# Kernel optimization log

Hardware: AMD Instinct MI355X
Metric: run time of the kernel (lower is better)

## Reference

```python
import jax, jax.numpy as jnp
import numpy as np

B, N, DIM, H, DH, K = 4, 2048, 512, 6, 64, 16
KEEP_PROB = 0.9  # 1 - dropout_rate
LOG2PI = float(np.log(2.0 * np.pi))
LOG_PRIOR = float(np.log(1.0 / K))


def setup_inputs() -> dict:
    key = jax.random.key(0)
    ks = jax.random.split(key, 7)
    inputs_q = jax.random.normal(ks[0], (B, N, DIM), dtype=jnp.float32)
    # decoder-style causal mask, shape [B, 1, q_len, kv_len]
    causal = jnp.tril(jnp.ones((N, N), dtype=jnp.float32))
    mask = jnp.broadcast_to(causal[None, None], (B, 1, N, N))
    # dropout keep mask broadcast across the query dim: [B, H, 1, kv_len]
    keep = jax.random.bernoulli(ks[1], KEEP_PROB, (B, H, 1, N)).astype(jnp.float32)
    w_qkv = jax.random.normal(ks[2], (DIM, 3 * H * DH), dtype=jnp.float32) * 0.02
    w_out = jax.random.normal(ks[3], (H * DH, DIM), dtype=jnp.float32) * 0.02
    mu_lookup = jax.random.normal(ks[4], (K, DIM), dtype=jnp.float32)
    logvar_lookup = jax.random.normal(ks[5], (K, DIM), dtype=jnp.float32) * 0.1
    return {
        "inputs_q": inputs_q,
        "mask": mask,
        "keep": keep,
        "w_qkv": w_qkv,
        "w_out": w_out,
        "mu_lookup": mu_lookup,
        "logvar_lookup": logvar_lookup,
    }


def reference(inputs_q, mask, keep, w_qkv, w_out, mu_lookup, logvar_lookup):
    # --- MultiHeadDotProductAttention (self-attn path) ---
    qkv = (inputs_q @ w_qkv).reshape(B, N, 3, H, DH)  # [B,N,3,H,DH]
    q, k, v = qkv[:, :, 0], qkv[:, :, 1], qkv[:, :, 2]
    # bias: 0 where mask > 0, -1e10 elsewhere (note: no 1/sqrt(d) scaling, as in source)
    bias = jnp.where(mask > 0, 0.0, -1e10)
    attn_weights = jnp.einsum('bqhd,bkhd->bhqk', q, k) + bias  # [B,H,N,N]
    attn_weights = jax.nn.softmax(attn_weights, axis=-1)
    # broadcast dropout: mask shared across the query dim
    attn_weights = attn_weights * keep / KEEP_PROB
    attn_out = jnp.einsum('bhqk,bkhd->bqhd', attn_weights, v)
    attn_out = attn_out.reshape(B, N, H * DH) @ w_out  # [B,N,DIM]

    # --- GMM posterior approx q(y|x) ~= p(y|z) (approx_qy_x, vectorized over k) ---
    z = attn_out.mean(axis=1)  # pooled latent, [B,DIM]
    diff = z[:, None, :] - mu_lookup[None]  # [B,K,DIM]
    llh = -0.5 * jnp.sum(
        diff * diff / jnp.exp(logvar_lookup)[None] + logvar_lookup[None] + LOG2PI,
        axis=-1,
    )  # [B,K]
    logLogit_qy_x = llh + LOG_PRIOR
    qy_x = jax.nn.softmax(logLogit_qy_x, axis=1)  # [B,K]

    # combine mixture mean back in so both branches are live in one output
    return attn_out + (qy_x @ mu_lookup)[:, None, :]
```

## Files before the change

### kernel.cpp

```cpp
#include <hip/hip_runtime.h>
#include <cstdint>
#include <cstddef>

#define NH 6
#define NSEQ 2048
#define DIMD 512
#define BATCH 4
#define HD 384
#define LOG2PI_F 1.8378770664093453f
#define LOG2E_F 1.4426950408889634f
#define M12L2_F (-17.312340490667562f)

typedef __attribute__((ext_vector_type(8))) short short8;
typedef __attribute__((ext_vector_type(8))) unsigned short ushort8;
typedef __attribute__((ext_vector_type(4))) unsigned short ushort4v;
typedef __attribute__((ext_vector_type(4))) float floatx4;

__device__ inline unsigned short f2bf(float f){
  unsigned int u = __float_as_uint(f);
  u += 0x7FFFu + ((u>>16)&1u);
  return (unsigned short)(u>>16);
}

__device__ inline float exp2_raw(float x){
  float r; asm("v_exp_f32 %0, %1" : "=v"(r) : "v"(x)); return r;
}

#define GLD16(gp, lp) __builtin_amdgcn_global_load_lds( \
  (const __attribute__((address_space(1))) void*)(gp), \
  (__attribute__((address_space(3))) void*)(lp), 16, 0, 0)

__device__ inline void wtrans_body(
    const float* __restrict__ src, unsigned short* __restrict__ dst,
    int R, int C, int bx, int by, unsigned short* Ls, int t)
{
  const int r = t>>2, c0 = (t&3)*16;
  const int d0 = by*64, n0 = bx*64;
  #pragma unroll
  for (int j=0;j<16;j+=4){
    floatx4 v = *(const floatx4*)(src + (size_t)(d0+r)*C + n0 + c0 + j);
    #pragma unroll
    for(int jj=0;jj<4;jj++) Ls[r*72 + c0+j+jj] = f2bf(v[jj]);
  }
  __syncthreads();
  #pragma unroll
  for (int j=0;j<16;j+=8){
    ushort8 o;
    #pragma unroll
    for(int jj=0;jj<8;jj++) o[jj] = Ls[(c0+j+jj)*72 + r];
    *(ushort8*)(dst + (size_t)(n0+r)*R + d0 + c0 + j) = o;
  }
}

__global__ __launch_bounds__(256) void prep(
    const float* __restrict__ xq, unsigned short* __restrict__ xbf,
    const float* __restrict__ w_qkv, unsigned short* __restrict__ wqT,
    const float* __restrict__ w_out, unsigned short* __restrict__ woT)
{
  __shared__ __attribute__((aligned(16))) unsigned short Ls[64*72];
  const int bid = blockIdx.x, t = threadIdx.x;
  if (bid < 4096){
    int i = bid*256 + t;
    floatx4 v = *(const floatx4*)(xq + (size_t)i*4);
    ushort4v r;
    #pragma unroll
    for(int j=0;j<4;j++) r[j] = f2bf(v[j]);
    *(ushort4v*)(xbf + (size_t)i*4) = r;
  } else if (bid < 4240){
    int rb = bid - 4096;
    wtrans_body(w_qkv, wqT, 512, 1152, rb%18, rb/18, Ls, t);
  } else {
    int rb = bid - 4240;
    wtrans_body(w_out, woT, 384, 512, rb%8, rb/8, Ls, t);
  }
}

__global__ __launch_bounds__(256) void gemm_qkv(
    const unsigned short* __restrict__ A,
    const unsigned short* __restrict__ Bt,
    const float* __restrict__ keep,
    unsigned short* __restrict__ Qo, unsigned short* __restrict__ Ko,
    unsigned short* __restrict__ Vt)
{
  __shared__ __attribute__((aligned(16))) unsigned short Cs[128*132];
  unsigned short* As = Cs;
  unsigned short* Bs = Cs + 128*64;
  const int tid = threadIdx.x;
  const int w = tid>>6, lane = tid&63;
  const int wr = w>>1, wc = w&1;
  const int quad = lane>>4, l16 = lane&15;
  const int tM = blockIdx.x*128, tN = blockIdx.y*128;
  const int r8 = lane>>3, c8 = (lane&7)*8;
  floatx4 acc[4][4];
  floatx4 zed = {0.f,0.f,0.f,0.f};
  #pragma unroll
  for (int i=0;i<4;i++)
    #pragma unroll
    for(int j=0;j<4;j++) acc[i][j] = zed;

  for (int k0=0; k0<512; k0+=64){
    #pragma unroll
    for (int i=0;i<4;i++){
      int row = w*32 + i*8;
      GLD16(A  + (size_t)(tM+row+r8)*512 + k0 + c8, As + row*64);
      GLD16(Bt + (size_t)(tN+row+r8)*512 + k0 + c8, Bs + row*64);
    }
    __syncthreads();
    #pragma unroll
    for (int kk=0; kk<64; kk+=32){
      short8 af[4], bf[4];
      #pragma unroll
      for(int mt=0;mt<4;mt++)
        af[mt] = *(const short8*)(As + (wr*64+mt*16+l16)*64 + kk + quad*8);
      #pragma unroll
      for(int nt=0;nt<4;nt++)
        bf[nt] = *(const short8*)(Bs + (wc*64+nt*16+l16)*64 + kk + quad*8);
      #pragma unroll
      for(int mt=0;mt<4;mt++)
        #pragma unroll
        for(int nt=0;nt<4;nt++)
          acc[mt][nt] = __builtin_amdgcn_mfma_f32_16x16x32_bf16(af[mt], bf[nt], acc[mt][nt], 0,0,0);
    }
    __syncthreads();
  }
  #pragma unroll
  for(int mt=0;mt<4;mt++)
    #pragma unroll
    for(int nt=0;nt<4;nt++){
      int gcol = tN + wc*64 + nt*16 + l16;
      float qs = (gcol < 384) ? LOG2E_F : 1.0f;
      #pragma unroll
      for(int r=0;r<4;r++)
        Cs[(wr*64+mt*16+quad*4+r)*132 + wc*64+nt*16+l16] = f2bf(acc[mt][nt][r]*qs);
    }
  __syncthreads();
  if (blockIdx.y < 6){
    const int row = tid>>1, colh = (tid&1)*64;
    const int gcol0 = tN + colh;
    const int t = gcol0/384, rem = gcol0 - t*384, h = rem>>6;
    const int grow = tM + row, b = grow>>11, n = grow & 2047;
    unsigned short* dst = (t==0 ? Qo : Ko) + ((size_t)((b*NH+h)*NSEQ+n))*64;
    #pragma unroll
    for(int j=0;j<8;j++)
      *(ushort8*)(dst + j*8) = *(const ushort8*)(Cs + row*132 + colh + j*8);
  } else {
    const int dcol = tid>>1;
    const int nh   = (tid&1)*64;
    const int gcol = tN + dcol;
    const int rem = gcol - 768, h = rem>>6, dh = rem&63;
    const int b = tM>>11, nb = tM & 2047;
    const float* kp = keep + (size_t)(b*NH+h)*NSEQ + nb + nh;
    unsigned short* dst = Vt + ((size_t)((b*NH+h)*64 + dh))*NSEQ + nb + nh;
    #pragma unroll
    for (int j8=0;j8<8;j8++){
      floatx4 k0 = *(const floatx4*)(kp + j8*8);
      floatx4 k1 = *(const floatx4*)(kp + j8*8 + 4);
      ushort8 o;
      #pragma unroll
      for(int u=0;u<4;u++)
        o[u]   = (k0[u] < 0.5f) ? (unsigned short)0 : Cs[(nh + j8*8 + u)*132 + dcol];
      #pragma unroll
      for(int u=0;u<4;u++)
        o[4+u] = (k1[u] < 0.5f) ? (unsigned short)0 : Cs[(nh + j8*8 + 4 + u)*132 + dcol];
      *(ushort8*)(dst + j8*8) = o;
    }
  }
}

__global__ __launch_bounds__(256, 3) void attn_kernel(
    const unsigned short* __restrict__ Qg, const unsigned short* __restrict__ Kg,
    const unsigned short* __restrict__ VtG,
    unsigned short* __restrict__ atp)
{
  __shared__ __attribute__((aligned(16))) float sm[4*32*34 + 128];
  float* Ocs  = sm;
  float* accs = sm + 4*32*34;
  const int tid = threadIdx.x;
  const int w = tid>>6, lane = tid&63;
  const int quad = lane>>4, l16 = lane&15;
  const int bid = blockIdx.x;
  const int idx = bid>>3;
  const int bh  = (bid&7) + 8*(idx % 3);
  const int c   = 63 - idx/3;
  const int b = bh/NH, h = bh - b*NH;
  const unsigned short* Qb = Qg  + (size_t)bh*NSEQ*64;
  const int q0 = c*32;
  const int nkt = (c>>1) + 1;
  const int q_abs0 = q0 + l16;

  const unsigned short* Kl = Kg  + (size_t)bh*NSEQ*64 + (size_t)l16*64 + quad*8;
  const unsigned short* Vl = VtG + (size_t)bh*64*NSEQ + (size_t)l16*NSEQ + quad*8;

  short8 qf[2][2];
  #pragma unroll
  for(int mt=0;mt<2;mt++)
    #pragma unroll
    for(int kc=0;kc<2;kc++)
      qf[mt][kc] = *(const short8*)(Qb + (size_t)(q0+mt*16+l16)*64 + kc*32 + quad*8);

  floatx4 O[2][4];
  float accl[2] = {0.f, 0.f};
  floatx4 zed = {0.f,0.f,0.f,0.f};
  floatx4 m12v = {M12L2_F, M12L2_F, M12L2_F, M12L2_F};
  #pragma unroll
  for(int mt=0;mt<2;mt++)
    #pragma unroll
    for(int dt=0;dt<4;dt++) O[mt][dt] = zed;

  for (int kt = w; kt < nkt; kt += 4){
    const int kB = kt*64;
    short8 vf[2][4];
    const unsigned short* vp0 = Vl + kB;
    #pragma unroll
    for(int kh=0;kh<2;kh++)
      #pragma unroll
      for(int dt=0;dt<4;dt++)
        vf[kh][dt] = *(const short8*)(vp0 + (size_t)dt*32768 + kh*32);

    floatx4 sacc[2][4];
    #pragma unroll
    for(int mt=0;mt<2;mt++)
      #pragma unroll
      for(int nt=0;nt<4;nt++) sacc[mt][nt] = m12v;
    const unsigned short* kp0 = Kl + (size_t)kt*4096;
    #pragma unroll
    for(int nt=0;nt<4;nt++){
      short8 kf0 = *(const short8*)(kp0 + nt*1024);
      short8 kf1 = *(const short8*)(kp0 + nt*1024 + 32);
      #pragma unroll
      for(int mt=0;mt<2;mt++){
        sacc[mt][nt] = __builtin_amdgcn_mfma_f32_16x16x32_bf16(kf0, qf[mt][0], sacc[mt][nt], 0,0,0);
        sacc[mt][nt] = __builtin_amdgcn_mfma_f32_16x16x32_bf16(kf1, qf[mt][1], sacc[mt][nt], 0,0,0);
      }
    }

    const bool dia = (kt == nkt-1);
    #pragma unroll
    for(int mt=0;mt<2;mt++){
      const int qa = q_abs0 + mt*16;
      unsigned int d0[4], d1[4];
      float rs = 0.f;
      #pragma unroll
      for(int nt=0;nt<4;nt++){
        const int key0 = kB + nt*16 + quad*4;
        float p0 = exp2_raw(sacc[mt][nt][0]);
        float p1 = exp2_raw(sacc[mt][nt][1]);
        float p2 = exp2_raw(sacc[mt][nt][2]);
        float p3 = exp2_raw(sacc[mt][nt][3]);
        if (dia){
          p0 = (key0   <= qa) ? p0 : 0.f;
          p1 = (key0+1 <= qa) ? p1 : 0.f;
          p2 = (key0+2 <= qa) ? p2 : 0.f;
          p3 = (key0+3 <= qa) ? p3 : 0.f;
        }
        rs += (p0+p1) + (p2+p3);
        asm("v_cvt_pk_bf16_f32 %0, %1, %2" : "=v"(d0[nt]) : "v"(p0), "v"(p1));
        asm("v_cvt_pk_bf16_f32 %0, %1, %2" : "=v"(d1[nt]) : "v"(p2), "v"(p3));
      }
      accl[mt] += rs;
      #pragma unroll
      for(int kh=0;kh<2;kh++){
        unsigned int x0 = d0[2*kh],   x1 = d1[2*kh];
        unsigned int y0 = d0[2*kh+1], y1 = d1[2*kh+1];
        asm("v_permlane32_swap_b32 %0, %1" : "+v"(x0), "+v"(y0));
        asm("v_permlane16_swap_b32 %0, %1" : "+v"(x0), "+v"(y0));
        asm("v_permlane32_swap_b32 %0, %1" : "+v"(x1), "+v"(y1));
        asm("v_permlane16_swap_b32 %0, %1" : "+v"(x1), "+v"(y1));
        union { unsigned int u[4]; short8 s; } cvt;
        cvt.u[0] = x0; cvt.u[1] = x1; cvt.u[2] = y0; cvt.u[3] = y1;
        short8 pf = cvt.s;
        #pragma unroll
        for(int dt=0;dt<4;dt++)
          O[mt][dt] = __builtin_amdgcn_mfma_f32_16x16x32_bf16(pf, vf[kh][dt], O[mt][dt], 0,0,0);
      }
    }
  }

  #pragma unroll
  for(int mt=0;mt<2;mt++){
    accl[mt] += __shfl_xor(accl[mt], 16, 64);
    accl[mt] += __shfl_xor(accl[mt], 32, 64);
  }
  if (quad == 0){
    accs[w*32 + l16]      = accl[0];
    accs[w*32 + 16 + l16] = accl[1];
  }

  const int orow = tid>>3, oc4 = (tid&7)*4;
  float sc2 = 0.f;
  #pragma unroll
  for (int h2=0; h2<2; ++h2){
    float* Ow = Ocs + w*(32*34);
    #pragma unroll
    for(int mt=0;mt<2;mt++)
      #pragma unroll
      for(int d2=0;d2<2;d2++){
        const int dt = h2*2 + d2;
        #pragma unroll
        for(int r=0;r<4;r++)
          Ow[(mt*16+quad*4+r)*34 + d2*16 + l16] = O[mt][dt][r];
      }
    __syncthreads();
    if (h2 == 0){
      float as = accs[orow] + accs[32+orow] + accs[64+orow] + accs[96+orow];
      sc2 = (1.0f/0.9f) / as;
    }
    float fv[4];
    #pragma unroll
    for(int j=0;j<4;j++) fv[j] = 0.f;
    #pragma unroll
    for(int s=0;s<4;s++){
      const float* p = Ocs + s*(32*34) + orow*34 + oc4;
      #pragma unroll
      for(int j=0;j<4;j++) fv[j] += p[j];
    }
    ushort4v o4;
    #pragma unroll
    for(int j=0;j<4;j++) o4[j] = f2bf(fv[j]*sc2);
    *(ushort4v*)(atp + ((size_t)(b*NSEQ + q0 + orow))*HD + h*64 + h2*32 + oc4) = o4;
    __syncthreads();
  }
}

__global__ __launch_bounds__(256) void gemm_proj(
    const unsigned short* __restrict__ A,
    const unsigned short* __restrict__ Bt,
    float* __restrict__ out,
    float* __restrict__ z)
{
  __shared__ __attribute__((aligned(16))) unsigned short As[128*64];
  __shared__ __attribute__((aligned(16))) unsigned short Bs[128*64];
  const int tid = threadIdx.x;
  const int w = tid>>6, lane = tid&63;
  const int wr = w>>1, wc = w&1;
  const int quad = lane>>4, l16 = lane&15;
  const int tM = blockIdx.x*128, tN = blockIdx.y*128;
  const int r8 = lane>>3, c8 = (lane&7)*8;
  floatx4 acc[4][4];
  floatx4 zed = {0.f,0.f,0.f,0.f};
  #pragma unroll
  for (int i=0;i<4;i++)
    #pragma unroll
    for(int j=0;j<4;j++) acc[i][j] = zed;

  for (int k0=0; k0<384; k0+=64){
    #pragma unroll
    for (int i=0;i<4;i++){
      int row = w*32 + i*8;
      GLD16(A  + (size_t)(tM+row+r8)*384 + k0 + c8, As + row*64);
      GLD16(Bt + (size_t)(tN+row+r8)*384 + k0 + c8, Bs + row*64);
    }
    __syncthreads();
    #pragma unroll
    for (int kk=0; kk<64; kk+=32){
      short8 af[4], bf[4];
      #pragma unroll
      for(int mt=0;mt<4;mt++)
        af[mt] = *(const short8*)(As + (wr*64+mt*16+l16)*64 + kk + quad*8);
      #pragma unroll
      for(int nt=0;nt<4;nt++)
        bf[nt] = *(const short8*)(Bs + (wc*64+nt*16+l16)*64 + kk + quad*8);
      #pragma unroll
      for(int mt=0;mt<4;mt++)
        #pragma unroll
        for(int nt=0;nt<4;nt++)
          acc[mt][nt] = __builtin_amdgcn_mfma_f32_16x16x32_bf16(af[mt], bf[nt], acc[mt][nt], 0,0,0);
    }
    __syncthreads();
  }
  #pragma unroll
  for(int mt=0;mt<4;mt++){
    int grow = tM + wr*64 + mt*16 + quad*4;
    #pragma unroll
    for(int nt=0;nt<4;nt++){
      int gcol = tN + wc*64 + nt*16 + l16;
      #pragma unroll
      for(int r=0;r<4;r++)
        out[(size_t)(grow+r)*512 + gcol] = acc[mt][nt][r];
    }
  }
  #pragma unroll
  for(int nt=0;nt<4;nt++){
    float s = 0.f;
    #pragma unroll
    for(int mt=0;mt<4;mt++)
      #pragma unroll
      for(int r=0;r<4;r++) s += acc[mt][nt][r];
    s += __shfl_xor(s, 16, 64);
    s += __shfl_xor(s, 32, 64);
    if (quad == 0){
      int gcol = tN + wc*64 + nt*16 + l16;
      atomicAdd(&z[(tM>>11)*DIMD + gcol], s);
    }
  }
}

__global__ __launch_bounds__(256) void gmm_kernel(
    const float* __restrict__ z, const float* __restrict__ mu,
    const float* __restrict__ lv, float* __restrict__ c)
{
  __shared__ float sh[16];
  __shared__ float qy[16];
  int tid = threadIdx.x;
  int k = tid>>4, li = tid&15;
  int b = blockIdx.x;
  float part = 0.f;
  for(int d=li; d<DIMD; d+=16){
    float zz = z[b*DIMD+d] * (1.0f/2048.0f);
    float m = mu[k*DIMD+d], l = lv[k*DIMD+d];
    float diff = zz - m;
    part += diff*diff*__expf(-l) + l + LOG2PI_F;
  }
  #pragma unroll
  for(int off=8;off>=1;off>>=1) part += __shfl_xor(part, off, 64);
  if (li==0) sh[k] = part;
  __syncthreads();
  if (tid<16){
    float logit = -0.5f*sh[tid];
    float mx = logit;
    #pragma unroll
    for(int off=8;off>=1;off>>=1) mx = fmaxf(mx, __shfl_xor(mx, off, 64));
    float e = __expf(logit-mx);
    float se = e;
    #pragma unroll
    for(int off=8;off>=1;off>>=1) se += __shfl_xor(se, off, 64);
    qy[tid] = e/se;
  }
  __syncthreads();
  for(int d=tid; d<DIMD; d+=256){
    float accv = 0.f;
    #pragma unroll
    for(int kk=0;kk<16;kk++) accv += qy[kk]*mu[kk*DIMD+d];
    c[b*DIMD+d] = accv;
  }
}

__global__ __launch_bounds__(256) void final_add(
    float* __restrict__ out, const float* __restrict__ c)
{
  size_t i = ((size_t)blockIdx.x*256 + threadIdx.x)*4;
  int d = (int)(i & 511);
  int b = (int)(i >> 20);
  floatx4 a = *(const floatx4*)(out + i);
  floatx4 cc = *(const floatx4*)(c + b*DIMD + d);
  *(floatx4*)(out + i) = a + cc;
}

extern "C" void kernel_launch(void* const* d_in, const int* in_sizes, int n_in,
                              void* d_out, int out_size, void* d_ws, size_t ws_size,
                              hipStream_t stream) {
  const float* inputs_q = (const float*)d_in[0];
  const float* keep  = (const float*)d_in[2];
  const float* w_qkv = (const float*)d_in[3];
  const float* w_out = (const float*)d_in[4];
  const float* mu    = (const float*)d_in[5];
  const float* lv    = (const float*)d_in[6];
  float* out = (float*)d_out;
  char* ws = (char*)d_ws;
  size_t off = 0;
  auto alloc = [&](size_t bytes){ void* p = ws + off; off += (bytes + 255) & ~(size_t)255; return p; };
  unsigned short* Qb  = (unsigned short*)alloc((size_t)24*2048*64*2);
  unsigned short* Kb  = (unsigned short*)alloc((size_t)24*2048*64*2);
  unsigned short* Vt  = (unsigned short*)alloc((size_t)24*64*2048*2);
  unsigned short* xbf = (unsigned short*)alloc((size_t)8192*512*2);
  unsigned short* wqT = (unsigned short*)alloc((size_t)1152*512*2);
  unsigned short* woT = (unsigned short*)alloc((size_t)512*384*2);
  unsigned short* atp = (unsigned short*)alloc((size_t)8192*384*2);
  float* z  = (float*)alloc((size_t)4*512*4);
  float* c  = (float*)alloc((size_t)4*512*4);

  hipMemsetAsync(z, 0, 4*512*4, stream);
  prep<<<4288, 256, 0, stream>>>(inputs_q, xbf, w_qkv, wqT, w_out, woT);
  gemm_qkv<<<dim3(64,9), 256, 0, stream>>>(xbf, wqT, keep, Qb, Kb, Vt);
  attn_kernel<<<1536, 256, 0, stream>>>(Qb, Kb, Vt, atp);
  gemm_proj<<<dim3(64,4), 256, 0, stream>>>(atp, woT, out, z);
  gmm_kernel<<<4, 256, 0, stream>>>(z, mu, lv, c);
  final_add<<<4096, 256, 0, stream>>>(out, c);
}
```

Baseline: 230.0 us.

## Fuse projection GEMM, GMM posterior and final add via cooperative grid sync

Merges gemm_proj, gmm_kernel and final_add into one cooperative kernel. After the projection accumulates the pooled z with atomics, a grid-wide sync lets every block compute the GMM softmax redundantly and add the mixture mean to its register accumulators before a single store. This removes the 32 MB output write-then-reread and two kernel launches. The z zeroing moves from a memset into prep. The cost is a grid barrier, redundant per-block GMM work, and a requirement that all 256 blocks be co-resident.

Result: slower. 254.2 us (+10.5%).

```diff
diff --git a/kernel.cpp b/kernel.cpp
--- a/kernel.cpp
+++ b/kernel.cpp
@@ -1,6 +1,9 @@
 #include <hip/hip_runtime.h>
+#include <hip/hip_cooperative_groups.h>
 #include <cstdint>
 #include <cstddef>
+
+namespace cg = cooperative_groups;
 
 #define NH 6
 #define NSEQ 2048
@@ -55,11 +58,16 @@
 __global__ __launch_bounds__(256) void prep(
     const float* __restrict__ xq, unsigned short* __restrict__ xbf,
     const float* __restrict__ w_qkv, unsigned short* __restrict__ wqT,
-    const float* __restrict__ w_out, unsigned short* __restrict__ woT)
+    const float* __restrict__ w_out, unsigned short* __restrict__ woT,
+    float* __restrict__ z)
 {
   __shared__ __attribute__((aligned(16))) unsigned short Ls[64*72];
   const int bid = blockIdx.x, t = threadIdx.x;
   if (bid < 4096){
+    if (bid == 0){
+      #pragma unroll
+      for(int j=0;j<8;j++) z[t*8+j] = 0.f;
+    }
     int i = bid*256 + t;
     floatx4 v = *(const floatx4*)(xq + (size_t)i*4);
     ushort4v r;
@@ -322,14 +330,18 @@
   }
 }
 
-__global__ __launch_bounds__(256) void gemm_proj(
+__global__ __launch_bounds__(256) void proj_gmm(
     const unsigned short* __restrict__ A,
     const unsigned short* __restrict__ Bt,
+    const float* __restrict__ mu,
+    const float* __restrict__ lv,
     float* __restrict__ out,
     float* __restrict__ z)
 {
   __shared__ __attribute__((aligned(16))) unsigned short As[128*64];
   __shared__ __attribute__((aligned(16))) unsigned short Bs[128*64];
+  __shared__ float sh[16];
+  __shared__ float qy[16];
   const int tid = threadIdx.x;
   const int w = tid>>6, lane = tid&63;
   const int wr = w>>1, wc = w&1;
@@ -368,17 +380,8 @@
     }
     __syncthreads();
   }
-  #pragma unroll
-  for(int mt=0;mt<4;mt++){
-    int grow = tM + wr*64 + mt*16 + quad*4;
-    #pragma unroll
-    for(int nt=0;nt<4;nt++){
-      int gcol = tN + wc*64 + nt*16 + l16;
-      #pragma unroll
-      for(int r=0;r<4;r++)
-        out[(size_t)(grow+r)*512 + gcol] = acc[mt][nt][r];
-    }
-  }
+
+  const int bq = tM>>11;
   #pragma unroll
   for(int nt=0;nt<4;nt++){
     float s = 0.f;
@@ -390,30 +393,25 @@
     s += __shfl_xor(s, 32, 64);
     if (quad == 0){
       int gcol = tN + wc*64 + nt*16 + l16;
-      atomicAdd(&z[(tM>>11)*DIMD + gcol], s);
-    }
-  }
-}
-
-__global__ __launch_bounds__(256) void gmm_kernel(
-    const float* __restrict__ z, const float* __restrict__ mu,
-    const float* __restrict__ lv, float* __restrict__ c)
-{
-  __shared__ float sh[16];
-  __shared__ float qy[16];
-  int tid = threadIdx.x;
-  int k = tid>>4, li = tid&15;
-  int b = blockIdx.x;
-  float part = 0.f;
-  for(int d=li; d<DIMD; d+=16){
-    float zz = z[b*DIMD+d] * (1.0f/2048.0f);
-    float m = mu[k*DIMD+d], l = lv[k*DIMD+d];
-    float diff = zz - m;
-    part += diff*diff*__expf(-l) + l + LOG2PI_F;
-  }
-  #pragma unroll
-  for(int off=8;off>=1;off>>=1) part += __shfl_xor(part, off, 64);
-  if (li==0) sh[k] = part;
+      atomicAdd(&z[bq*DIMD + gcol], s);
+    }
+  }
+
+  cg::this_grid().sync();
+
+  {
+    const int k = tid>>4, li = tid&15;
+    float part = 0.f;
+    for(int d=li; d<DIMD; d+=16){
+      float zz = z[bq*DIMD+d] * (1.0f/2048.0f);
+      float m = mu[k*DIMD+d], l = lv[k*DIMD+d];
+      float diff = zz - m;
+      part += diff*diff*__expf(-l) + l + LOG2PI_F;
+    }
+    #pragma unroll
+    for(int off=8;off>=1;off>>=1) part += __shfl_xor(part, off, 64);
+    if (li==0) sh[k] = part;
+  }
   __syncthreads();
   if (tid<16){
     float logit = -0.5f*sh[tid];
@@ -427,23 +425,21 @@
     qy[tid] = e/se;
   }
   __syncthreads();
-  for(int d=tid; d<DIMD; d+=256){
-    float accv = 0.f;
-    #pragma unroll
-    for(int kk=0;kk<16;kk++) accv += qy[kk]*mu[kk*DIMD+d];
-    c[b*DIMD+d] = accv;
-  }
-}
-
-__global__ __launch_bounds__(256) void final_add(
-    float* __restrict__ out, const float* __restrict__ c)
-{
-  size_t i = ((size_t)blockIdx.x*256 + threadIdx.x)*4;
-  int d = (int)(i & 511);
-  int b = (int)(i >> 20);
-  floatx4 a = *(const floatx4*)(out + i);
-  floatx4 cc = *(const floatx4*)(c + b*DIMD + d);
-  *(floatx4*)(out + i) = a + cc;
+
+  #pragma unroll
+  for(int nt=0;nt<4;nt++){
+    const int gcol = tN + wc*64 + nt*16 + l16;
+    float cc = 0.f;
+    #pragma unroll
+    for(int kk=0;kk<16;kk++) cc += qy[kk]*mu[kk*DIMD+gcol];
+    #pragma unroll
+    for(int mt=0;mt<4;mt++){
+      const int grow = tM + wr*64 + mt*16 + quad*4;
+      #pragma unroll
+      for(int r=0;r<4;r++)
+        out[(size_t)(grow+r)*512 + gcol] = acc[mt][nt][r] + cc;
+    }
+  }
 }
 
 extern "C" void kernel_launch(void* const* d_in, const int* in_sizes, int n_in,
@@ -467,13 +463,15 @@
   unsigned short* woT = (unsigned short*)alloc((size_t)512*384*2);
   unsigned short* atp = (unsigned short*)alloc((size_t)8192*384*2);
   float* z  = (float*)alloc((size_t)4*512*4);
-  float* c  = (float*)alloc((size_t)4*512*4);
-
-  hipMemsetAsync(z, 0, 4*512*4, stream);
-  prep<<<4288, 256, 0, stream>>>(inputs_q, xbf, w_qkv, wqT, w_out, woT);
+
+  prep<<<4288, 256, 0, stream>>>(inputs_q, xbf, w_qkv, wqT, w_out, woT, z);
   gemm_qkv<<<dim3(64,9), 256, 0, stream>>>(xbf, wqT, keep, Qb, Kb, Vt);
   attn_kernel<<<1536, 256, 0, stream>>>(Qb, Kb, Vt, atp);
-  gemm_proj<<<dim3(64,4), 256, 0, stream>>>(atp, woT, out, z);
-  gmm_kernel<<<4, 256, 0, stream>>>(z, mu, lv, c);
-  final_add<<<4096, 256, 0, stream>>>(out, c);
-}
+
+  const unsigned short* atp_c = atp;
+  const unsigned short* woT_c = woT;
+  void* args[] = { (void*)&atp_c, (void*)&woT_c, (void*)&mu, (void*)&lv,
+                   (void*)&out, (void*)&z };
+  hipLaunchCooperativeKernel((void*)proj_gmm, dim3(64,4), dim3(256),
+                             args, 0, stream);
+}
```
